# Kernel tuning notes

Measured on AMD Instinct MI355X. Metric: run time of the kernel, lower is better.

Reference implementation:

```python
import jax, jax.numpy as jnp
import numpy as np

B, IMG_ROWS, TSTEPS = 64, 32, 128
HID, CIN = 64, 512  # ncde hidden, ncde input dim = 32 * (IMG_ROWS//2)


def _linear(x, w, b):
    return x @ w.T + b


def _conv(x, w, b, pad):
    y = jax.lax.conv_general_dilated(x, w, (1, 1), [(pad, pad), (pad, pad)],
                                     dimension_numbers=('NCHW', 'OIHW', 'NCHW'))
    return y + b[None, :, None, None]


def _maxpool2(x):
    return jax.lax.reduce_window(x, -jnp.inf, jax.lax.max, (1, 1, 2, 2), (1, 1, 2, 2), 'VALID')


def _natural_cubic_coeffs(x):
    # x: [B, L, C], uniform knots t=0..L-1 (h=1). Natural cubic spline.
    L = x.shape[1]
    n = L - 2
    A = 4.0 * jnp.eye(n, dtype=x.dtype) + jnp.eye(n, k=1, dtype=x.dtype) + jnp.eye(n, k=-1, dtype=x.dtype)
    rhs = 6.0 * (x[:, 2:] - 2.0 * x[:, 1:-1] + x[:, :-2])  # [B, n, C]
    Mi = jnp.linalg.solve(A, rhs.transpose(1, 0, 2).reshape(n, -1))
    Mi = Mi.reshape(n, x.shape[0], x.shape[2]).transpose(1, 0, 2)
    M = jnp.pad(Mi, ((0, 0), (1, 1), (0, 0)))  # natural BCs: M0 = M_{L-1} = 0
    a = x[:, :-1]
    b = (x[:, 1:] - x[:, :-1]) - (2.0 * M[:, :-1] + M[:, 1:]) / 6.0
    c = M[:, :-1] / 2.0
    d = (M[:, 1:] - M[:, :-1]) / 6.0
    return a, b, c, d  # each [B, L-1, C]


def _forward(x, conv1_w, conv1_b, conv2_w, conv2_b, att_fc1_w, att_fc1_b,
             att_fc2_w, att_fc2_b, initial_w, initial_b, f1_w, f1_b,
             f2_w, f2_b, out_w, out_b):
    h = jax.nn.relu(_conv(x, conv1_w, conv1_b, pad=2))
    h = jax.nn.relu(_conv(h, conv2_w, conv2_b, pad=1))
    h = _maxpool2(h)  # [B,32,16,T/2]  (dropout is identity in eval)
    att = h.mean(axis=(2, 3))  # AdaptiveAvgPool2d(1)
    att = jax.nn.sigmoid(_linear(jax.nn.relu(_linear(att, att_fc1_w, att_fc1_b)), att_fc2_w, att_fc2_b))
    h = h * att[:, :, None, None]
    h = jnp.transpose(h, (0, 3, 1, 2))
    seq = h.reshape(h.shape[0], h.shape[1], -1)  # [B, L, 512]
    L = seq.shape[1]
    _, sb, sc, sd = _natural_cubic_coeffs(seq)

    z0 = _linear(seq[:, 0], initial_w, initial_b)  # spline.evaluate(t0) == seq[:,0]

    def cdefunc(z):
        u = jax.nn.relu(_linear(z, f1_w, f1_b))
        u = jnp.tanh(_linear(u, f2_w, f2_b))
        return u.reshape(z.shape[0], HID, CIN)

    def dXdt(t):
        seg = jnp.clip(jnp.floor(t).astype(jnp.int32), 0, L - 2)
        fr = t - seg.astype(t.dtype)
        return sb[:, seg] + 2.0 * sc[:, seg] * fr + 3.0 * sd[:, seg] * fr * fr

    def vf(t, z):
        return jnp.einsum('bhc,bc->bh', cdefunc(z), dXdt(t))

    dt = jnp.float32(0.5)
    nsteps = 2 * (L - 1)

    @jax.checkpoint
    def step(z, t):
        k1 = vf(t, z)
        k2 = vf(t + dt / 2, z + dt / 2 * k1)
        k3 = vf(t + dt / 2, z + dt / 2 * k2)
        k4 = vf(t + dt, z + dt * k3)
        return z + dt / 6.0 * (k1 + 2 * k2 + 2 * k3 + k4), None

    ts = jnp.arange(nsteps, dtype=jnp.float32) * dt
    zT, _ = jax.lax.scan(step, z0, ts)
    return _linear(zT, out_w, out_b)


def setup_inputs() -> dict:
    key = jax.random.key(0)
    ks = jax.random.split(key, 10)
    s = lambda k, shape, sc=0.05: (jax.random.normal(k, shape, jnp.float32) * sc)
    z = lambda n: jnp.zeros((n,), jnp.float32)
    return {
        'x': jax.random.normal(ks[0], (B, 1, IMG_ROWS, TSTEPS), jnp.float32),
        'conv1_w': s(ks[1], (32, 1, 5, 5)), 'conv1_b': z(32),
        'conv2_w': s(ks[2], (32, 32, 3, 3)), 'conv2_b': z(32),
        'att_fc1_w': s(ks[3], (4, 32)), 'att_fc1_b': z(4),
        'att_fc2_w': s(ks[4], (32, 4)), 'att_fc2_b': z(32),
        'initial_w': s(ks[5], (HID, CIN)), 'initial_b': z(HID),
        'f1_w': s(ks[6], (128, HID)), 'f1_b': z(128),
        'f2_w': s(ks[7], (CIN * HID, 128)), 'f2_b': z(CIN * HID),
        'out_w': s(ks[8], (2, HID)), 'out_b': z(2),
    }


def reference(x, conv1_w, conv1_b, conv2_w, conv2_b, att_fc1_w, att_fc1_b,
              att_fc2_w, att_fc2_b, initial_w, initial_b, f1_w, f1_b,
              f2_w, f2_b, out_w, out_b):
    return _forward(x, conv1_w, conv1_b, conv2_w, conv2_b, att_fc1_w, att_fc1_b,
                    att_fc2_w, att_fc2_b, initial_w, initial_b, f1_w, f1_b,
                    f2_w, f2_b, out_w, out_b)
```

## Files before the change

kernel.cpp:

```cpp
#include <hip/hip_runtime.h>
#include <hip/hip_bf16.h>
#include <stdint.h>

#define NSTEP 126
#define NEVAL 504
#define POISON 0xAAAAAAAAu

typedef __bf16 v8bf __attribute__((ext_vector_type(8)));
typedef float  v4f  __attribute__((ext_vector_type(4)));

__device__ __forceinline__ unsigned short f2bf(float x) {
  union { float f; uint32_t u; } v; v.f = x;
  uint32_t u = v.u;
  uint32_t r = (u + 0x7FFFu + ((u >> 16) & 1u)) >> 16;
  return (unsigned short)r;
}
__device__ __forceinline__ float bf2f(unsigned short b) {
  union { uint32_t u; float f; } v; v.u = ((uint32_t)b) << 16;
  return v.f;
}
__device__ __forceinline__ uint32_t cvt_pk_bf16(float lo, float hi) {
  uint32_t r;
  asm("v_cvt_pk_bf16_f32 %0, %1, %2" : "=v"(r) : "v"(lo), "v"(hi));
  return r;
}

#define LDA(p) __hip_atomic_load((p), __ATOMIC_RELAXED, __HIP_MEMORY_SCOPE_AGENT)

#define BARL() asm volatile("s_waitcnt lgkmcnt(0)\n\ts_barrier" ::: "memory")

__global__ void k_detect(const uint32_t* __restrict__ xw, int* flag) {
  __shared__ int cnt;
  if (threadIdx.x == 0) cnt = 0;
  __syncthreads();
  uint32_t w = xw[threadIdx.x];
  int e = (int)((w >> 7) & 0xFF);
  int good = ((e >= 100) && (e <= 144)) || ((w & 0xFFFFu) == 0u);
  atomicAdd(&cnt, good);
  __syncthreads();
  if (threadIdx.x == 0) *flag = (cnt >= 192) ? 1 : 0;
}

#define NCVT 15
struct CvtArgs {
  const void* src[NCVT];
  int dstoff[NCVT];
  int len[NCVT];
  int kind[NCVT];
  int total;
};
__global__ void k_convert(CvtArgs a, float* __restrict__ ws, const int* __restrict__ flag) {
  int f = *flag;
  for (int i = blockIdx.x*256 + threadIdx.x; i < a.total; i += gridDim.x*256) {
    int t = 0; int rem = i;
    while (rem >= a.len[t]) { rem -= a.len[t]; t++; }
    float v = f ? bf2f(((const unsigned short*)a.src[t])[rem])
                : ((const float*)a.src[t])[rem];
    int d;
    if (a.kind[t] == 1) { int h = rem >> 9, c = rem & 511; d = a.dstoff[t] + c*64 + h; }
    else if (a.kind[t] == 2) {
      int co = rem / 288, r2 = rem % 288;
      int ci = r2 / 9, tt = r2 % 9;
      d = a.dstoff[t] + (co >> 4)*4608 + (ci*16 + (co & 15))*9 + tt;
    }
    else d = a.dstoff[t] + rem;
    ws[d] = v;
  }
}

__global__ void k_wbf16(const void* __restrict__ w2src, const void* __restrict__ w1src,
                        unsigned short* __restrict__ w2bf, unsigned short* __restrict__ w1bf,
                        const int* __restrict__ flag) {
  int f = *flag;
  const long N2 = 4194304, N1 = 8192;
  for (long i = (long)blockIdx.x*256 + threadIdx.x; i < N2 + N1; i += (long)gridDim.x*256) {
    if (i < N2) w2bf[i] = f ? ((const unsigned short*)w2src)[i] : f2bf(((const float*)w2src)[i]);
    else { long j = i - N2; w1bf[j] = f ? ((const unsigned short*)w1src)[j] : f2bf(((const float*)w1src)[j]); }
  }
}

__global__ void k_conv1(const float* __restrict__ xf, const float* __restrict__ w,
                        const float* __restrict__ bias, float* __restrict__ h1) {
  int x = threadIdx.x;
  int y = blockIdx.x;
  int b = blockIdx.y;
  const float* xin = xf + (long)b*4096;
  float in[25];
  #pragma unroll
  for (int ky = 0; ky < 5; ky++) {
    int yy = y + ky - 2;
    #pragma unroll
    for (int kx = 0; kx < 5; kx++) {
      int xx = x + kx - 2;
      in[ky*5+kx] = (yy >= 0 && yy < 32 && xx >= 0 && xx < 128) ? xin[yy*128 + xx] : 0.f;
    }
  }
  for (int co = 0; co < 32; co++) {
    float acc = bias[co];
    #pragma unroll
    for (int t = 0; t < 25; t++) acc += in[t] * w[co*25 + t];
    h1[(((long)b*32 + co)*32 + y)*128 + x] = fmaxf(acc, 0.f);
  }
}

#define LD2 132
__global__ __launch_bounds__(256) void k_conv2(const float* __restrict__ h1, const float* __restrict__ w,
                                               const float* __restrict__ bias, float* __restrict__ h2) {
  __shared__ float s[32][3][LD2];
  int y = blockIdx.x, b = blockIdx.y;
  int tid = threadIdx.x;
  for (int i = tid; i < 32*3*LD2; i += 256) {
    int ci = i / (3*LD2);
    int r  = (i / LD2) % 3;
    int xx = i % LD2;
    int yy = y + r - 1, sx = xx - 1;
    float v = 0.f;
    if (yy >= 0 && yy < 32 && sx >= 0 && sx < 128) v = h1[(((long)b*32+ci)*32+yy)*128+sx];
    s[ci][r][xx] = v;
  }
  __syncthreads();
  int x = tid & 127;
  int half = __builtin_amdgcn_readfirstlane(tid >> 7);
  const float* wb = w + half*4608;
  float acc[16];
  #pragma unroll
  for (int i = 0; i < 16; i++) acc[i] = bias[half*16 + i];
  #pragma unroll 2
  for (int ci = 0; ci < 32; ci++) {
    float xv[9];
    #pragma unroll
    for (int r = 0; r < 3; r++)
      #pragma unroll
      for (int k = 0; k < 3; k++) xv[r*3+k] = s[ci][r][x + k];
    #pragma unroll
    for (int co = 0; co < 16; co++) {
      const float* wr = wb + (ci*16 + co)*9;
      #pragma unroll
      for (int t = 0; t < 9; t++) acc[co] += xv[t] * wr[t];
    }
  }
  #pragma unroll
  for (int co = 0; co < 16; co++)
    h2[(((long)b*32 + half*16 + co)*32 + y)*128 + x] = fmaxf(acc[co], 0.f);
}

__global__ void k_pool(const float* __restrict__ h2, float* __restrict__ pooled, float* __restrict__ attm) {
  int bc = blockIdx.x;
  const float* src = h2 + (long)bc*4096;
  float* dst = pooled + (long)bc*1024;
  float sum = 0.f;
  for (int i = threadIdx.x; i < 1024; i += 256) {
    int py = i >> 6, px = i & 63;
    const float* p = src + py*256 + px*2;
    float m = fmaxf(fmaxf(p[0], p[1]), fmaxf(p[128], p[129]));
    dst[i] = m;
    sum += m;
  }
  __shared__ float red[256];
  red[threadIdx.x] = sum;
  __syncthreads();
  for (int s2 = 128; s2 > 0; s2 >>= 1) {
    if (threadIdx.x < s2) red[threadIdx.x] += red[threadIdx.x + s2];
    __syncthreads();
  }
  if (threadIdx.x == 0) attm[bc] = red[0] * (1.f/1024.f);
}

__global__ void k_att(const float* __restrict__ attm, const float* __restrict__ w1, const float* __restrict__ b1,
                      const float* __restrict__ w2, const float* __restrict__ b2, float* __restrict__ atts) {
  int b = threadIdx.x;
  if (b < 64) {
    float hb[4];
    #pragma unroll
    for (int j = 0; j < 4; j++) {
      float s = b1[j];
      for (int i = 0; i < 32; i++) s += attm[b*32+i]*w1[j*32+i];
      hb[j] = fmaxf(s, 0.f);
    }
    for (int o = 0; o < 32; o++) {
      float s = b2[o];
      #pragma unroll
      for (int j = 0; j < 4; j++) s += hb[j]*w2[o*4+j];
      atts[b*32+o] = 1.f/(1.f + __expf(-s));
    }
  }
}

__global__ void k_seq(const float* __restrict__ pooled, const float* __restrict__ atts, float* __restrict__ seq) {
  for (int idx = blockIdx.x*256 + threadIdx.x; idx < 64*64*512; idx += gridDim.x*256) {
    int b = idx >> 15;
    int t = (idx >> 9) & 63;
    int fch = idx & 511;
    int c = fch >> 4, hh = fch & 15;
    seq[idx] = pooled[(((long)b*32 + c)*16 + hh)*64 + t] * atts[b*32 + c];
  }
}

__global__ __launch_bounds__(256, 1) void k_spline(const float* __restrict__ seq,
                                                   float* __restrict__ dxt) {
  int id = blockIdx.x*256 + threadIdx.x;
  int b = id >> 9, f = id & 511;
  const float* xp = seq + (long)b*32768 + f;
  float xv[64];
  #pragma unroll
  for (int t = 0; t < 64; t++) xv[t] = xp[t*512];
  float cp[62], dp[62];
  float pc = 0.f, pd = 0.f;
  #pragma unroll
  for (int i = 0; i < 62; i++) {
    float rhs = 6.f*(xv[i+2] - 2.f*xv[i+1] + xv[i]);
    float inv = 1.f/(4.f - pc);
    pc = inv;
    pd = (rhs - pd)*inv;
    cp[i] = pc; dp[i] = pd;
  }
  #pragma unroll
  for (int i = 60; i >= 0; i--) dp[i] = dp[i] - cp[i]*dp[i+1];
  const float i6 = 1.f/6.f;
  float* op = dxt + (long)b*512 + f;
  #pragma unroll
  for (int t = 0; t < 63; t++) {
    float M0 = (t == 0)  ? 0.f : dp[t-1];
    float M1 = (t == 62) ? 0.f : dp[t];
    float sb = (xv[t+1] - xv[t]) - (2.f*M0 + M1)*i6;
    float sc = 0.5f*M0;
    float sd = (M1 - M0)*i6;
    float* o = op + (long)(4*t)*32768;
    o[0]      = sb;
    o[32768]  = sb + 0.5f*sc + 0.1875f*sd;
    o[65536]  = sb + sc + 0.75f*sd;
    o[98304]  = sb + 1.5f*sc + 1.6875f*sd;
    if (t == 62) o[131072] = sb + 2.f*sc + 3.f*sd;
  }
}

__global__ void k_z0(const float* __restrict__ seq, const float* __restrict__ iwT,
                     const float* __restrict__ ib, float* __restrict__ z0) {
  __shared__ float s0[512];
  int b = blockIdx.x, h = threadIdx.x;
  for (int c = h; c < 512; c += 64) s0[c] = seq[(long)b*32768 + c];
  __syncthreads();
  float acc = ib[h];
  for (int c = 0; c < 512; c++) acc += s0[c]*iwT[c*64 + h];
  z0[b*64 + h] = acc;
}

__global__ __launch_bounds__(512, 2) void k_ode(
    const float* __restrict__ z0buf,
    const unsigned short* __restrict__ w2bf,
    const unsigned short* __restrict__ w1bf,
    const float* __restrict__ f1bias,
    const float* __restrict__ f2bias,
    const float* __restrict__ dxt,
    const float* __restrict__ outw,
    const float* __restrict__ outb,
    uint32_t* kpart,
    void* dout,
    const int* __restrict__ flag)
{
  __shared__ __align__(16) unsigned short zs[16*72];
  __shared__ __align__(16) unsigned short ub[16*136];
  __shared__ __align__(16) float dxs[16*524 + 10560];
  __shared__ float kred[128];

  int tid = threadIdx.x;
  int bl  = blockIdx.x;
  int hb  = bl >> 2;
  int bq  = bl & 3;
  int B0  = bq*16;
  int lane = tid & 63, wv = tid >> 6;
  int q = lane >> 4, ln = lane & 15;

  v8bf w2f[4][4];
  #pragma unroll
  for (int jt = 0; jt < 4; jt++)
    #pragma unroll
    for (int ks = 0; ks < 4; ks++) {
      long row = (long)hb*512 + wv*64 + jt*16 + ln;
      w2f[jt][ks] = *(const v8bf*)(w2bf + row*128 + ks*32 + q*8);
    }
  v8bf w1f[2];
  #pragma unroll
  for (int ks = 0; ks < 2; ks++)
    w1f[ks] = *(const v8bf*)(w1bf + (wv*16 + ln)*64 + ks*32 + q*8);
  float fb2[4][4];
  #pragma unroll
  for (int jt = 0; jt < 4; jt++)
    #pragma unroll
    for (int r = 0; r < 4; r++)
      fb2[jt][r] = f2bias[(long)hb*512 + wv*64 + jt*16 + q*4 + r];
  float fb1[4];
  #pragma unroll
  for (int r = 0; r < 4; r++)
    fb1[r] = f1bias[wv*16 + q*4 + r];

  int zbL = tid & 15;
  int hg  = tid >> 4;
  int h0  = hg*2;
  float z[2], zacc[2];
  #pragma unroll
  for (int i = 0; i < 2; i++) { z[i] = z0buf[(B0+zbL)*64 + h0 + i]; zacc[i] = 0.f; }

  v4f dxc[4];
  const float dt6 = 0.5f/6.f;
  int e = 0;
  for (int step = 0; step < NSTEP; step++) {
    #pragma unroll 1
    for (int stage = 0; stage < 4; stage++, e++) {
      bool do_dx = (stage == 1) || (stage == 3) || (e == 0);
      int m = 2*step + ((stage + 1) >> 1);
      if (do_dx) {
        const float* dxb = dxt + (long)m*32768 + (B0+ln)*512 + wv*64 + q*4;
        #pragma unroll
        for (int jt = 0; jt < 4; jt++)
          dxc[jt] = *(const v4f*)(dxb + jt*16);
      }
      if (e > 0) {
        const uint32_t* kp = kpart + ((long)(e-1)*4 + bq)*1024;
        uint32_t kvu[2];
        const uint32_t* p0 = kp + (h0+0)*16 + zbL;
        const uint32_t* p1 = kp + (h0+1)*16 + zbL;
        kvu[0] = LDA(p0);
        kvu[1] = LDA(p1);
        while (kvu[0] == POISON) {
          __builtin_amdgcn_s_sleep(1);
          kvu[0] = LDA(p0);
        }
        while (kvu[1] == POISON) {
          __builtin_amdgcn_s_sleep(1);
          kvu[1] = LDA(p1);
        }
        float kv0 = __uint_as_float(kvu[0]);
        float kv1 = __uint_as_float(kvu[1]);
        if (stage == 0) {
          z[0] += dt6*(zacc[0] + kv0);
          z[1] += dt6*(zacc[1] + kv1);
          zacc[0] = 0.f; zacc[1] = 0.f;
          *(uint32_t*)(zs + zbL*72 + h0) = cvt_pk_bf16(z[0], z[1]);
        } else {
          float wk = (stage == 1) ? 1.f : 2.f;
          float aa = (stage == 3) ? 0.5f : 0.25f;
          zacc[0] += wk*kv0;
          zacc[1] += wk*kv1;
          *(uint32_t*)(zs + zbL*72 + h0) = cvt_pk_bf16(z[0] + aa*kv0, z[1] + aa*kv1);
        }
      } else {
        *(uint32_t*)(zs + zbL*72 + h0) = cvt_pk_bf16(z[0], z[1]);
      }
      BARL();
      v8bf zf[2];
      #pragma unroll
      for (int ks = 0; ks < 2; ks++)
        zf[ks] = *(const v8bf*)(zs + ln*72 + ks*32 + q*8);
      {
        v4f ua = (v4f){fb1[0], fb1[1], fb1[2], fb1[3]};
        #pragma unroll
        for (int ks = 0; ks < 2; ks++)
          ua = __builtin_amdgcn_mfma_f32_16x16x32_bf16(w1f[ks], zf[ks], ua, 0, 0, 0);
        uint2 upk;
        upk.x = cvt_pk_bf16(fmaxf(ua[0], 0.f), fmaxf(ua[1], 0.f));
        upk.y = cvt_pk_bf16(fmaxf(ua[2], 0.f), fmaxf(ua[3], 0.f));
        *(uint2*)(ub + ln*136 + wv*16 + q*4) = upk;
      }
      BARL();
      v8bf uf[4];
      #pragma unroll
      for (int ks = 0; ks < 4; ks++)
        uf[ks] = *(const v8bf*)(ub + ln*136 + ks*32 + q*8);
      float ksum = 0.f;
      #pragma unroll
      for (int jt = 0; jt < 4; jt++) {
        v4f acc = (v4f){fb2[jt][0], fb2[jt][1], fb2[jt][2], fb2[jt][3]};
        #pragma unroll
        for (int ks = 0; ks < 4; ks++)
          acc = __builtin_amdgcn_mfma_f32_16x16x32_bf16(w2f[jt][ks], uf[ks], acc, 0, 0, 0);
        v4f dx4 = dxc[jt];
        #pragma unroll
        for (int r = 0; r < 4; r++) {
          float xv2 = acc[r];
          float ex = __expf(2.f*xv2);
          float th = 1.f - 2.f*__builtin_amdgcn_rcpf(ex + 1.f);
          ksum += th*dx4[r];
        }
      }
      ksum += __shfl_xor(ksum, 16, 64);
      ksum += __shfl_xor(ksum, 32, 64);
      if (lane < 16)
        kred[ln*8 + wv] = ksum;
      BARL();
      if (tid < 16) {
        const float* kr = kred + tid*8;
        float v = ((((((kr[0]+kr[1])+kr[2])+kr[3])+kr[4])+kr[5])+kr[6])+kr[7];
        uint32_t uv = __float_as_uint(v);
        if (uv == POISON) uv ^= 1u;
        __hip_atomic_store(kpart + (((long)e*4 + bq)*64 + hb)*16 + tid, uv,
                           __ATOMIC_RELAXED, __HIP_MEMORY_SCOPE_AGENT);
      }
    }
  }
  if (hb == 0) {
    const uint32_t* kp = kpart + ((long)(NEVAL-1)*4 + bq)*1024;
    {
      #pragma unroll
      for (int i = 0; i < 2; i++) {
        const uint32_t* p = kp + (h0+i)*16 + zbL;
        uint32_t v = LDA(p);
        while (v == POISON) {
          __builtin_amdgcn_s_sleep(1);
          v = LDA(p);
        }
        z[i] += dt6*(zacc[i] + __uint_as_float(v));
      }
    }
    float o0 = z[0]*outw[h0] + z[1]*outw[h0+1];
    float o1 = z[0]*outw[64+h0] + z[1]*outw[64+h0+1];
    __syncthreads();
    dxs[hg*32 + zbL*2 + 0] = o0;
    dxs[hg*32 + zbL*2 + 1] = o1;
    __syncthreads();
    if (tid < 32) {
      int bloc = tid >> 1, comp = tid & 1;
      float s = outb[comp];
      #pragma unroll
      for (int g = 0; g < 32; g++) s += dxs[g*32 + bloc*2 + comp];
      int b = B0 + bloc;
      if (*flag) ((unsigned short*)dout)[b*2 + comp] = f2bf(s);
      else       ((float*)dout)[b*2 + comp] = s;
    }
  }
}

extern "C" void kernel_launch(void* const* d_in, const int* in_sizes, int n_in,
                              void* d_out, int out_size, void* d_ws, size_t ws_size,
                              hipStream_t stream) {
  (void)in_sizes; (void)n_in; (void)out_size; (void)ws_size;
  float* ws = (float*)d_ws;
  size_t o = 0;
  auto alloc = [&](size_t n) { size_t r = o; o += (n + 63) & ~(size_t)63; return r; };
  size_t o_flag = alloc(64);
  size_t o_xf   = alloc(262144);
  size_t o_c1w  = alloc(800);
  size_t o_c1b  = alloc(32);
  size_t o_c2w  = alloc(9216);
  size_t o_c2b  = alloc(32);
  size_t o_a1w  = alloc(128);
  size_t o_a1b  = alloc(4);
  size_t o_a2w  = alloc(128);
  size_t o_a2b  = alloc(32);
  size_t o_iwT  = alloc(32768);
  size_t o_ib   = alloc(64);
  size_t o_f1b  = alloc(128);
  size_t o_f2b  = alloc(32768);
  size_t o_ow   = alloc(128);
  size_t o_ob   = alloc(2);
  size_t o_z0   = alloc(4096);
  size_t o_attm = alloc(2048);
  size_t o_atts = alloc(2048);
  size_t o_w1bf = alloc(4096);
  size_t o_w2bf = alloc(2097152);
  size_t o_h1   = alloc(8388608);
  size_t o_h2   = alloc(8388608);
  size_t o_kpart= alloc(4128768);
  size_t o_pool = o_h1;
  size_t o_seq  = o_h1 + 2097152;
  size_t o_dxt  = o_h2;

  int* flag = (int*)(ws + o_flag);

  hipLaunchKernelGGL(k_detect, dim3(1), dim3(256), 0, stream, (const uint32_t*)d_in[0], flag);

  CvtArgs ca;
  const int  si[NCVT]  = {0,1,2,3,4,5,6,7,8,9,10,12,14,15,16};
  const size_t dofs[NCVT] = {o_xf,o_c1w,o_c1b,o_c2w,o_c2b,o_a1w,o_a1b,o_a2w,o_a2b,o_iwT,o_ib,o_f1b,o_f2b,o_ow,o_ob};
  const int  ln[NCVT]  = {262144,800,32,9216,32,128,4,128,32,32768,64,128,32768,128,2};
  int tot = 0;
  for (int i = 0; i < NCVT; i++) {
    ca.src[i] = d_in[si[i]];
    ca.dstoff[i] = (int)dofs[i];
    ca.len[i] = ln[i];
    ca.kind[i] = (si[i] == 9) ? 1 : ((si[i] == 3) ? 2 : 0);
    tot += ln[i];
  }
  ca.total = tot;
  hipLaunchKernelGGL(k_convert, dim3(512), dim3(256), 0, stream, ca, ws, flag);
  hipLaunchKernelGGL(k_wbf16, dim3(2048), dim3(256), 0, stream, d_in[13], d_in[11],
                     (unsigned short*)(ws + o_w2bf), (unsigned short*)(ws + o_w1bf), flag);
  hipLaunchKernelGGL(k_conv1, dim3(32,64), dim3(128), 0, stream, ws+o_xf, ws+o_c1w, ws+o_c1b, ws+o_h1);
  hipLaunchKernelGGL(k_conv2, dim3(32,64), dim3(256), 0, stream, ws+o_h1, ws+o_c2w, ws+o_c2b, ws+o_h2);
  hipLaunchKernelGGL(k_pool, dim3(2048), dim3(256), 0, stream, ws+o_h2, ws+o_pool, ws+o_attm);
  hipLaunchKernelGGL(k_att, dim3(1), dim3(64), 0, stream, ws+o_attm, ws+o_a1w, ws+o_a1b, ws+o_a2w, ws+o_a2b, ws+o_atts);
  hipLaunchKernelGGL(k_seq, dim3(2048), dim3(256), 0, stream, ws+o_pool, ws+o_atts, ws+o_seq);
  hipLaunchKernelGGL(k_spline, dim3(128), dim3(256), 0, stream, ws+o_seq, ws+o_dxt);
  hipLaunchKernelGGL(k_z0, dim3(64), dim3(64), 0, stream, ws+o_seq, ws+o_iwT, ws+o_ib, ws+o_z0);

  hipLaunchKernelGGL(k_ode, dim3(256), dim3(512), 0, stream,
                     ws + o_z0,
                     (const unsigned short*)(ws + o_w2bf),
                     (const unsigned short*)(ws + o_w1bf),
                     ws + o_f1b, ws + o_f2b,
                     ws + o_dxt, ws + o_ow, ws + o_ob,
                     (uint32_t*)(ws + o_kpart),
                     d_out, (const int*)flag);
}
```

Measured before the change: 1.458 ms.

## Double ODE block width to 1024 threads, halving per-wave f2 tile work

The persistent ODE kernel now launches 1024 threads per block instead of 512. Each wave owns 32 output rows of the f2 weight slice rather than 64, so register-held weights, biases and dx fragments are halved, and each thread tracks one hidden state instead of two. The first-layer MFMA runs only on the first 8 waves, and the cross-wave reduction sums 16 partials. The aim is more waves in flight to hide the MFMA, tanh and dx-load latency on the serial RK4 critical path. The cost is a larger barrier group and a longer reduction on every stage.

```diff
diff --git a/kernel.cpp b/kernel.cpp
--- a/kernel.cpp
+++ b/kernel.cpp
@@ -245,7 +245,7 @@
   z0[b*64 + h] = acc;
 }
 
-__global__ __launch_bounds__(512, 2) void k_ode(
+__global__ __launch_bounds__(1024, 4) void k_ode(
     const float* __restrict__ z0buf,
     const unsigned short* __restrict__ w2bf,
     const unsigned short* __restrict__ w1bf,
@@ -260,8 +260,8 @@
 {
   __shared__ __align__(16) unsigned short zs[16*72];
   __shared__ __align__(16) unsigned short ub[16*136];
-  __shared__ __align__(16) float dxs[16*524 + 10560];
-  __shared__ float kred[128];
+  __shared__ __align__(16) float dxs[19200];
+  __shared__ float kred[256];
 
   int tid = threadIdx.x;
   int bl  = blockIdx.x;
@@ -270,38 +270,37 @@
   int B0  = bq*16;
   int lane = tid & 63, wv = tid >> 6;
   int q = lane >> 4, ln = lane & 15;
-
-  v8bf w2f[4][4];
-  #pragma unroll
-  for (int jt = 0; jt < 4; jt++)
+  int wv8 = wv & 7;
+
+  v8bf w2f[2][4];
+  #pragma unroll
+  for (int jt = 0; jt < 2; jt++)
     #pragma unroll
     for (int ks = 0; ks < 4; ks++) {
-      long row = (long)hb*512 + wv*64 + jt*16 + ln;
+      long row = (long)hb*512 + wv*32 + jt*16 + ln;
       w2f[jt][ks] = *(const v8bf*)(w2bf + row*128 + ks*32 + q*8);
     }
   v8bf w1f[2];
   #pragma unroll
   for (int ks = 0; ks < 2; ks++)
-    w1f[ks] = *(const v8bf*)(w1bf + (wv*16 + ln)*64 + ks*32 + q*8);
-  float fb2[4][4];
-  #pragma unroll
-  for (int jt = 0; jt < 4; jt++)
+    w1f[ks] = *(const v8bf*)(w1bf + (wv8*16 + ln)*64 + ks*32 + q*8);
+  float fb2[2][4];
+  #pragma unroll
+  for (int jt = 0; jt < 2; jt++)
     #pragma unroll
     for (int r = 0; r < 4; r++)
-      fb2[jt][r] = f2bias[(long)hb*512 + wv*64 + jt*16 + q*4 + r];
+      fb2[jt][r] = f2bias[(long)hb*512 + wv*32 + jt*16 + q*4 + r];
   float fb1[4];
   #pragma unroll
   for (int r = 0; r < 4; r++)
-    fb1[r] = f1bias[wv*16 + q*4 + r];
+    fb1[r] = f1bias[wv8*16 + q*4 + r];
 
   int zbL = tid & 15;
-  int hg  = tid >> 4;
-  int h0  = hg*2;
-  float z[2], zacc[2];
-  #pragma unroll
-  for (int i = 0; i < 2; i++) { z[i] = z0buf[(B0+zbL)*64 + h0 + i]; zacc[i] = 0.f; }
-
-  v4f dxc[4];
+  int h0  = tid >> 4;
+  float z = z0buf[(B0+zbL)*64 + h0];
+  float zacc = 0.f;
+
+  v4f dxc[2];
   const float dt6 = 0.5f/6.f;
   int e = 0;
   for (int step = 0; step < NSTEP; step++) {
@@ -310,49 +309,44 @@
       bool do_dx = (stage == 1) || (stage == 3) || (e == 0);
       int m = 2*step + ((stage + 1) >> 1);
       if (do_dx) {
-        const float* dxb = dxt + (long)m*32768 + (B0+ln)*512 + wv*64 + q*4;
-        #pragma unroll
-        for (int jt = 0; jt < 4; jt++)
-          dxc[jt] = *(const v4f*)(dxb + jt*16);
-      }
+        const float* dxb = dxt + (long)m*32768 + (B0+ln)*512 + wv*32 + q*4;
+        dxc[0] = *(const v4f*)(dxb);
+        dxc[1] = *(const v4f*)(dxb + 16);
+      }
+      float zw;
       if (e > 0) {
         const uint32_t* kp = kpart + ((long)(e-1)*4 + bq)*1024;
-        uint32_t kvu[2];
-        const uint32_t* p0 = kp + (h0+0)*16 + zbL;
-        const uint32_t* p1 = kp + (h0+1)*16 + zbL;
-        kvu[0] = LDA(p0);
-        kvu[1] = LDA(p1);
-        while (kvu[0] == POISON) {
+        const uint32_t* p0 = kp + h0*16 + zbL;
+        uint32_t kvu = LDA(p0);
+        while (kvu == POISON) {
           __builtin_amdgcn_s_sleep(1);
-          kvu[0] = LDA(p0);
+          kvu = LDA(p0);
         }
-        while (kvu[1] == POISON) {
-          __builtin_amdgcn_s_sleep(1);
-          kvu[1] = LDA(p1);
-        }
-        float kv0 = __uint_as_float(kvu[0]);
-        float kv1 = __uint_as_float(kvu[1]);
+        float kv = __uint_as_float(kvu);
         if (stage == 0) {
-          z[0] += dt6*(zacc[0] + kv0);
-          z[1] += dt6*(zacc[1] + kv1);
-          zacc[0] = 0.f; zacc[1] = 0.f;
-          *(uint32_t*)(zs + zbL*72 + h0) = cvt_pk_bf16(z[0], z[1]);
+          z += dt6*(zacc + kv);
+          zacc = 0.f;
+          zw = z;
         } else {
           float wk = (stage == 1) ? 1.f : 2.f;
           float aa = (stage == 3) ? 0.5f : 0.25f;
-          zacc[0] += wk*kv0;
-          zacc[1] += wk*kv1;
-          *(uint32_t*)(zs + zbL*72 + h0) = cvt_pk_bf16(z[0] + aa*kv0, z[1] + aa*kv1);
+          zacc += wk*kv;
+          zw = z + aa*kv;
         }
       } else {
-        *(uint32_t*)(zs + zbL*72 + h0) = cvt_pk_bf16(z[0], z[1]);
+        zw = z;
+      }
+      {
+        float zp = __shfl_xor(zw, 16, 64);
+        if ((h0 & 1) == 0)
+          *(uint32_t*)(zs + zbL*72 + h0) = cvt_pk_bf16(zw, zp);
       }
       BARL();
-      v8bf zf[2];
-      #pragma unroll
-      for (int ks = 0; ks < 2; ks++)
-        zf[ks] = *(const v8bf*)(zs + ln*72 + ks*32 + q*8);
-      {
+      if (wv < 8) {
+        v8bf zf[2];
+        #pragma unroll
+        for (int ks = 0; ks < 2; ks++)
+          zf[ks] = *(const v8bf*)(zs + ln*72 + ks*32 + q*8);
         v4f ua = (v4f){fb1[0], fb1[1], fb1[2], fb1[3]};
         #pragma unroll
         for (int ks = 0; ks < 2; ks++)
@@ -360,7 +354,7 @@
         uint2 upk;
         upk.x = cvt_pk_bf16(fmaxf(ua[0], 0.f), fmaxf(ua[1], 0.f));
         upk.y = cvt_pk_bf16(fmaxf(ua[2], 0.f), fmaxf(ua[3], 0.f));
-        *(uint2*)(ub + ln*136 + wv*16 + q*4) = upk;
+        *(uint2*)(ub + ln*136 + wv8*16 + q*4) = upk;
       }
       BARL();
       v8bf uf[4];
@@ -369,7 +363,7 @@
         uf[ks] = *(const v8bf*)(ub + ln*136 + ks*32 + q*8);
       float ksum = 0.f;
       #pragma unroll
-      for (int jt = 0; jt < 4; jt++) {
+      for (int jt = 0; jt < 2; jt++) {
         v4f acc = (v4f){fb2[jt][0], fb2[jt][1], fb2[jt][2], fb2[jt][3]};
         #pragma unroll
         for (int ks = 0; ks < 4; ks++)
@@ -386,11 +380,13 @@
       ksum += __shfl_xor(ksum, 16, 64);
       ksum += __shfl_xor(ksum, 32, 64);
       if (lane < 16)
-        kred[ln*8 + wv] = ksum;
+        kred[ln*16 + wv] = ksum;
       BARL();
       if (tid < 16) {
-        const float* kr = kred + tid*8;
-        float v = ((((((kr[0]+kr[1])+kr[2])+kr[3])+kr[4])+kr[5])+kr[6])+kr[7];
+        const float* kr = kred + tid*16;
+        float s0 = ((kr[0]+kr[1]) + (kr[2]+kr[3])) + ((kr[4]+kr[5]) + (kr[6]+kr[7]));
+        float s1 = ((kr[8]+kr[9]) + (kr[10]+kr[11])) + ((kr[12]+kr[13]) + (kr[14]+kr[15]));
+        float v = s0 + s1;
         uint32_t uv = __float_as_uint(v);
         if (uv == POISON) uv ^= 1u;
         __hip_atomic_store(kpart + (((long)e*4 + bq)*64 + hb)*16 + tid, uv,
@@ -401,28 +397,25 @@
   if (hb == 0) {
     const uint32_t* kp = kpart + ((long)(NEVAL-1)*4 + bq)*1024;
     {
-      #pragma unroll
-      for (int i = 0; i < 2; i++) {
-        const uint32_t* p = kp + (h0+i)*16 + zbL;
-        uint32_t v = LDA(p);
-        while (v == POISON) {
-          __builtin_amdgcn_s_sleep(1);
-          v = LDA(p);
-        }
-        z[i] += dt6*(zacc[i] + __uint_as_float(v));
-      }
-    }
-    float o0 = z[0]*outw[h0] + z[1]*outw[h0+1];
-    float o1 = z[0]*outw[64+h0] + z[1]*outw[64+h0+1];
+      const uint32_t* p = kp + h0*16 + zbL;
+      uint32_t v = LDA(p);
+      while (v == POISON) {
+        __builtin_amdgcn_s_sleep(1);
+        v = LDA(p);
+      }
+      z += dt6*(zacc + __uint_as_float(v));
+    }
+    float o0 = z*outw[h0];
+    float o1 = z*outw[64+h0];
     __syncthreads();
-    dxs[hg*32 + zbL*2 + 0] = o0;
-    dxs[hg*32 + zbL*2 + 1] = o1;
+    dxs[h0*32 + zbL*2 + 0] = o0;
+    dxs[h0*32 + zbL*2 + 1] = o1;
     __syncthreads();
     if (tid < 32) {
       int bloc = tid >> 1, comp = tid & 1;
       float s = outb[comp];
       #pragma unroll
-      for (int g = 0; g < 32; g++) s += dxs[g*32 + bloc*2 + comp];
+      for (int g = 0; g < 64; g++) s += dxs[g*32 + bloc*2 + comp];
       int b = B0 + bloc;
       if (*flag) ((unsigned short*)dout)[b*2 + comp] = f2bf(s);
       else       ((float*)dout)[b*2 + comp] = s;
@@ -493,7 +486,7 @@
   hipLaunchKernelGGL(k_spline, dim3(128), dim3(256), 0, stream, ws+o_seq, ws+o_dxt);
   hipLaunchKernelGGL(k_z0, dim3(64), dim3(64), 0, stream, ws+o_seq, ws+o_iwT, ws+o_ib, ws+o_z0);
 
-  hipLaunchKernelGGL(k_ode, dim3(256), dim3(512), 0, stream,
+  hipLaunchKernelGGL(k_ode, dim3(256), dim3(1024), 0, stream,
                      ws + o_z0,
                      (const unsigned short*)(ws + o_w2bf),
                      (const unsigned short*)(ws + o_w1bf),
```

Measured after the change: 1.494 ms. +2.4%, slower.
